# Kernel tuning notes

Hardware: AMD Instinct MI355X
Metric: run time of the kernel (lower is better)

The kernel has to match this reference:

```python
import jax, jax.numpy as jnp
import numpy as np

B, N_PER, D, L, DEG = 16, 2048, 128, 4, 16
N = B * N_PER
E = N * DEG
MSG_EPS = 1e-7  # GENConv message eps


def _lin_init(k, fi, fo):
    kw, kb = jax.random.split(k)
    s = 1.0 / np.sqrt(fi)
    W = jax.random.uniform(kw, (fi, fo), jnp.float32, minval=-s, maxval=s)
    b = jax.random.uniform(kb, (fo,), jnp.float32, minval=-s, maxval=s)
    return W, b


def setup_inputs() -> dict:
    key = jax.random.key(0)
    ks = jax.random.split(key, 6 + 2 * L)
    flat_c = jax.random.normal(ks[0], (N,), jnp.float32)
    edge_weight = jax.random.normal(ks[1], (E,), jnp.float32)
    # edges confined within each graph: local indices + per-graph offset
    e_per = N_PER * DEG
    local = jax.random.randint(ks[2], (2, B, e_per), 0, N_PER, jnp.int32)
    offs = (jnp.arange(B, dtype=jnp.int32) * N_PER)[None, :, None]
    edge_index = (local + offs).reshape(2, E)
    node_W, node_b = _lin_init(ks[3], 1, D)
    edge_W, edge_b = _lin_init(ks[4], 1, D)
    W1l, b1l, W2l, b2l = [], [], [], []
    for i in range(L):
        w1, bb1 = _lin_init(ks[6 + 2 * i], D, 2 * D)
        w2, bb2 = _lin_init(ks[7 + 2 * i], 2 * D, D)
        W1l.append(w1); b1l.append(bb1); W2l.append(w2); b2l.append(bb2)
    lin_W, lin_b = _lin_init(ks[5], D, 1)
    return dict(
        flat_c=flat_c, edge_weight=edge_weight, edge_index=edge_index,
        node_W=node_W, node_b=node_b, edge_W=edge_W, edge_b=edge_b,
        ts=jnp.ones((L,), jnp.float32),
        W1=jnp.stack(W1l), b1=jnp.stack(b1l),
        g1=jnp.ones((L, 2 * D), jnp.float32), be1=jnp.zeros((L, 2 * D), jnp.float32),
        W2=jnp.stack(W2l), b2=jnp.stack(b2l),
        ln_g=jnp.ones((L, D), jnp.float32), ln_b=jnp.zeros((L, D), jnp.float32),
        lin_W=lin_W, lin_b=lin_b)


def _layernorm(x, g, b, eps=1e-5):
    mu = jnp.mean(x, -1, keepdims=True)
    var = jnp.mean((x - mu) ** 2, -1, keepdims=True)
    return (x - mu) * jax.lax.rsqrt(var + eps) * g + b


def _gen_conv(x, edge_attr, src, dst, t, W1, b1, g1, be1, W2, b2):
    # GENConv with softmax aggregation (per-destination, per-channel)
    m = jax.nn.relu(x[src] + edge_attr) + MSG_EPS          # [E, D]
    logits = m * t
    mx = jax.ops.segment_max(logits, dst, num_segments=N)  # [N, D]
    ex = jnp.exp(logits - mx[dst])
    denom = jax.ops.segment_sum(ex, dst, num_segments=N)
    alpha = ex / (denom[dst] + 1e-16)
    aggr = jax.ops.segment_sum(m * alpha, dst, num_segments=N)  # [N, D]
    h = aggr + x
    # MLP: Linear(D,2D) -> LayerNorm -> ReLU -> Linear(2D,D)
    h = jax.nn.relu(_layernorm(h @ W1 + b1, g1, be1))
    return h @ W2 + b2


def reference(flat_c, edge_weight, edge_index, node_W, node_b, edge_W, edge_b,
              ts, W1, b1, g1, be1, W2, b2, ln_g, ln_b, lin_W, lin_b):
    src, dst = edge_index[0], edge_index[1]
    x = flat_c[:, None] @ node_W + node_b              # [N, D]
    ea = edge_weight[:, None] @ edge_W + edge_b        # [E, D]
    # first layer: raw conv only (pre-activation 'res+' scheme)
    x = _gen_conv(x, ea, src, dst, ts[0], W1[0], b1[0], g1[0], be1[0], W2[0], b2[0])
    for l in range(1, L):
        h = x
        z = jax.nn.relu(_layernorm(x, ln_g[l], ln_b[l]))  # dropout=identity (eval)
        x = _gen_conv(z, ea, src, dst, ts[l], W1[l], b1[l], g1[l], be1[l], W2[l], b2[l]) + h
    x = jax.nn.relu(_layernorm(x, ln_g[0], ln_b[0]))
    x = x @ lin_W + lin_b                              # [N, 1]
    out = x.reshape(B, N_PER)                          # equal-size graphs, max_len = N_PER
    return out - out[:, :1]                            # subtract first-node output per graph
```

## Files before the change

kernel.cpp:

```cpp
#include <hip/hip_runtime.h>
#include <hip/hip_bf16.h>
#include <stdint.h>

#define NN   32768
#define EE   524288
#define DD   128
#define D2   256
#define NPER 2048

using f32x4 = __attribute__((ext_vector_type(4))) float;
using sh8   = __attribute__((ext_vector_type(8))) short;
using sh4   = __attribute__((ext_vector_type(4))) short;

__device__ inline uint32_t rtn_hi_bits(float x){
  uint32_t u = __float_as_uint(x);
  return (u + 0x7FFFu + ((u >> 16) & 1u)) & 0xFFFF0000u;
}

__device__ inline int swz_node(int blk, int wave){
  int s = (blk & 7) * 1024 + (blk >> 3);
  return s * 4 + wave;
}

__global__ void k_count(const int* __restrict__ dst, int* __restrict__ cnt){
  int e = blockIdx.x * 256 + threadIdx.x;
  if (e < EE) atomicAdd(&cnt[dst[e]], 1);
}

__global__ __launch_bounds__(1024)
void k_scan(const int* __restrict__ cnt, int* __restrict__ rowptr){
  __shared__ int ps[1024];
  int t = threadIdx.x;
  int loc[32];
  int base = t * 32;
  int s = 0;
  #pragma unroll
  for (int j = 0; j < 32; ++j){ loc[j] = cnt[base + j]; s += loc[j]; }
  ps[t] = s; __syncthreads();
  for (int off = 1; off < 1024; off <<= 1){
    int v = (t >= off) ? ps[t - off] : 0;
    __syncthreads();
    ps[t] += v;
    __syncthreads();
  }
  int run = ps[t] - s;
  #pragma unroll
  for (int j = 0; j < 32; ++j){ rowptr[base + j] = run; run += loc[j]; }
  if (t == 1023) rowptr[NN] = run;
}

__global__ void k_scatter(const int* __restrict__ src, const int* __restrict__ dst,
                          const float* __restrict__ w, const int* __restrict__ rowptr,
                          int* __restrict__ cur, int* __restrict__ es, float* __restrict__ ew){
  int e = blockIdx.x * 256 + threadIdx.x;
  if (e < EE){
    int d = dst[e];
    int pos = rowptr[d] + atomicAdd(&cur[d], 1);
    es[pos] = src[e];
    ew[pos] = w[e];
  }
}

__global__ __launch_bounds__(256)
void k_packw1(const float* __restrict__ W1, ushort* __restrict__ Wh, ushort* __restrict__ Wl){
  int t = blockIdx.x * 256 + threadIdx.x;
  int lane = t & 63, mt = (t >> 6) & 15, kt = (t >> 10) & 3, layer = t >> 12;
  int nl = lane & 15, g = lane >> 4;
  int ucol = mt * 16 + nl;
  const float* Wp = W1 + layer * (DD * D2);
  sh8 hh, ll;
  #pragma unroll
  for (int j = 0; j < 8; ++j){
    int k = kt * 32 + g * 4 + (j & 3) + 16 * (j >> 2);
    float v = Wp[k * D2 + ucol];
    uint32_t hb = rtn_hi_bits(v);
    hh[j] = (short)(hb >> 16);
    ll[j] = (short)(__float_as_uint(v - __uint_as_float(hb)) >> 16);
  }
  *(sh8*)(Wh + t * 8) = hh;
  *(sh8*)(Wl + t * 8) = ll;
}

__global__ __launch_bounds__(256)
void k_packw2(const float* __restrict__ W2, ushort* __restrict__ Wh, ushort* __restrict__ Wl){
  int t = blockIdx.x * 256 + threadIdx.x;
  int lane = t & 63, mt = (t >> 6) & 7, kt = (t >> 9) & 7, layer = t >> 12;
  int nl = lane & 15, g = lane >> 4;
  int xcol = mt * 16 + nl;
  const float* Wp = W2 + layer * (D2 * DD);
  sh8 hh, ll;
  #pragma unroll
  for (int j = 0; j < 8; ++j){
    int k = kt * 32 + g * 4 + (j & 3) + 16 * (j >> 2);
    float v = Wp[k * DD + xcol];
    uint32_t hb = rtn_hi_bits(v);
    hh[j] = (short)(hb >> 16);
    ll[j] = (short)(__float_as_uint(v - __uint_as_float(hb)) >> 16);
  }
  *(sh8*)(Wh + t * 8) = hh;
  *(sh8*)(Wl + t * 8) = ll;
}

__global__ __launch_bounds__(256)
void k_encode(const float* __restrict__ c, const float* __restrict__ nW,
              const float* __restrict__ nb, float* __restrict__ Z){
  int n  = swz_node(blockIdx.x, threadIdx.x >> 6);
  int d0 = (threadIdx.x & 63) * 2;
  float cv = c[n];
  float2 o;
  o.x = cv * nW[d0]     + nb[d0];
  o.y = cv * nW[d0 + 1] + nb[d0 + 1];
  *(float2*)(Z + (size_t)n * DD + d0) = o;
}

__global__ __launch_bounds__(256)
void k_edge(const float* __restrict__ Z, const int* __restrict__ rowptr,
            const int* __restrict__ es, const float* __restrict__ ew,
            const float* __restrict__ eW, const float* __restrict__ eB,
            const float* __restrict__ ts, int layer,
            ushort* __restrict__ Hh, ushort* __restrict__ Hl){
  int n  = swz_node(blockIdx.x, threadIdx.x >> 6);
  int ld = threadIdx.x & 63;
  int d0 = ld * 2;
  float t  = ts[layer];
  float wx = eW[d0], wy = eW[d0 + 1];
  float bx = eB[d0], by = eB[d0 + 1];
  int r0 = rowptr[n], r1 = rowptr[n + 1];
  int deg = r1 - r0;
  int dcap = deg < 64 ? deg : 64;

  int   se = 0; float we = 0.f;
  if (ld < deg){ se = es[r0 + ld]; we = ew[r0 + ld]; }

  float m0r = -1e30f, m1r = -1e30f;
  float s0a = 0.f, s1a = 0.f, a0a = 0.f, a1a = 0.f;

  auto body = [&](float2 zc, float wj){
    float m0 = fmaxf(zc.x + fmaf(wj, wx, bx), 0.f) + 1e-7f;
    float m1 = fmaxf(zc.y + fmaf(wj, wy, by), 0.f) + 1e-7f;
    float l0 = m0 * t, l1 = m1 * t;
    if (__builtin_expect(l0 > m0r + 8.f || l1 > m1r + 8.f, 0)){
      float n0 = fmaxf(m0r, l0), n1 = fmaxf(m1r, l1);
      float e0 = __expf(m0r - n0), e1 = __expf(m1r - n1);
      s0a *= e0; a0a *= e0; m0r = n0;
      s1a *= e1; a1a *= e1; m1r = n1;
    }
    float p0 = __expf(l0 - m0r), p1 = __expf(l1 - m1r);
    s0a += p0; a0a = fmaf(p0, m0, a0a);
    s1a += p1; a1a = fmaf(p1, m1, a1a);
  };

  float2 z0 = make_float2(0.f, 0.f), z1 = make_float2(0.f, 0.f);
  float  wA = 0.f, wB = 0.f;
  if (dcap > 0){
    int s0i = __shfl(se, 0); wA = __shfl(we, 0);
    z0 = *(const float2*)(Z + (size_t)s0i * DD + d0);
  }
  if (dcap > 1){
    int s1i = __shfl(se, 1); wB = __shfl(we, 1);
    z1 = *(const float2*)(Z + (size_t)s1i * DD + d0);
  }
  for (int j = 0; j < dcap; ++j){
    float2 zc = z0; float wj = wA;
    z0 = z1; wA = wB;
    if (j + 2 < dcap){
      int sn = __shfl(se, j + 2); wB = __shfl(we, j + 2);
      z1 = *(const float2*)(Z + (size_t)sn * DD + d0);
    }
    body(zc, wj);
  }
  for (int e = r0 + 64; e < r1; ++e){
    int   s = es[e];
    float w = ew[e];
    float2 zc = *(const float2*)(Z + (size_t)s * DD + d0);
    body(zc, w);
  }

  float2 zn = *(const float2*)(Z + (size_t)n * DD + d0);
  float hx = a0a / (s0a + 1e-16f) + zn.x;
  float hy = a1a / (s1a + 1e-16f) + zn.y;
  uint32_t hbx = rtn_hi_bits(hx), hby = rtn_hi_bits(hy);
  uint32_t hw = (hbx >> 16) | (hby & 0xFFFF0000u);
  float lx = hx - __uint_as_float(hbx), ly = hy - __uint_as_float(hby);
  uint32_t lw = (__float_as_uint(lx) >> 16) | (__float_as_uint(ly) & 0xFFFF0000u);
  ((uint32_t*)(Hh + (size_t)n * DD))[ld] = hw;
  ((uint32_t*)(Hl + (size_t)n * DD))[ld] = lw;
}

__global__ __launch_bounds__(256, 2)
void k_mlp(const ushort* __restrict__ Hhi, const ushort* __restrict__ Hlo,
           const ushort* __restrict__ W1h, const ushort* __restrict__ W1l,
           const float* __restrict__ b1, const float* __restrict__ g1,
           const float* __restrict__ be1,
           const ushort* __restrict__ W2h, const ushort* __restrict__ W2l,
           const float* __restrict__ b2, const float* __restrict__ Xres,
           float* __restrict__ Xout,
           const float* __restrict__ lnG, const float* __restrict__ lnB,
           float* __restrict__ Zout, int hasRes, int writeX)
{
  __shared__ ushort Ufh[16384];
  __shared__ ushort Ufl[16384];
  __shared__ float2 Pln[256];

  const int tid = threadIdx.x;
  const int w = tid >> 6, l = tid & 63, nl = l & 15, g = l >> 4;
  const int bs = (blockIdx.x & 7) * 64 + (blockIdx.x >> 3);
  const int n0 = bs * 64;

  f32x4 acc[4][4];
  #pragma unroll
  for (int mi = 0; mi < 4; ++mi)
    #pragma unroll
    for (int nt = 0; nt < 4; ++nt) acc[mi][nt] = (f32x4)0.f;

  const int hbase = (n0 + nl) * DD + g * 4;

  #pragma unroll
  for (int kt = 0; kt < 4; ++kt){
    sh8 ah[4], al[4];
    #pragma unroll
    for (int mi = 0; mi < 4; ++mi){
      int fi = ((kt * 16 + w * 4 + mi) * 64 + l) * 8;
      ah[mi] = *(const sh8*)(W1h + fi);
      al[mi] = *(const sh8*)(W1l + fi);
    }
    sh8 bh[4], bl[4];
    #pragma unroll
    for (int nt = 0; nt < 4; ++nt){
      int hi_ = hbase + nt * 16 * DD + kt * 32;
      sh8 vh, vl;
      ((sh4*)&vh)[0] = *(const sh4*)(Hhi + hi_);
      ((sh4*)&vh)[1] = *(const sh4*)(Hhi + hi_ + 16);
      ((sh4*)&vl)[0] = *(const sh4*)(Hlo + hi_);
      ((sh4*)&vl)[1] = *(const sh4*)(Hlo + hi_ + 16);
      bh[nt] = vh; bl[nt] = vl;
    }
    #pragma unroll
    for (int mi = 0; mi < 4; ++mi)
      #pragma unroll
      for (int nt = 0; nt < 4; ++nt){
        acc[mi][nt] = __builtin_amdgcn_mfma_f32_16x16x32_bf16(ah[mi], bh[nt], acc[mi][nt], 0, 0, 0);
        acc[mi][nt] = __builtin_amdgcn_mfma_f32_16x16x32_bf16(ah[mi], bl[nt], acc[mi][nt], 0, 0, 0);
        acc[mi][nt] = __builtin_amdgcn_mfma_f32_16x16x32_bf16(al[mi], bh[nt], acc[mi][nt], 0, 0, 0);
      }
  }

  #pragma unroll
  for (int mi = 0; mi < 4; ++mi){
    f32x4 bv = *(const f32x4*)(b1 + w * 64 + mi * 16 + g * 4);
    #pragma unroll
    for (int nt = 0; nt < 4; ++nt) acc[mi][nt] += bv;
  }
  float s1[4], s2[4];
  #pragma unroll
  for (int nt = 0; nt < 4; ++nt){
    float a = 0.f, b = 0.f;
    #pragma unroll
    for (int mi = 0; mi < 4; ++mi)
      #pragma unroll
      for (int r = 0; r < 4; ++r){ float v = acc[mi][nt][r]; a += v; b += v * v; }
    a += __shfl_xor(a, 16); b += __shfl_xor(b, 16);
    a += __shfl_xor(a, 32); b += __shfl_xor(b, 32);
    s1[nt] = a; s2[nt] = b;
  }
  {
    float p1 = (g == 0) ? s1[0] : (g == 1) ? s1[1] : (g == 2) ? s1[2] : s1[3];
    float p2 = (g == 0) ? s2[0] : (g == 1) ? s2[1] : (g == 2) ? s2[2] : s2[3];
    Pln[(g * 16 + nl) * 4 + w] = make_float2(p1, p2);
  }
  __syncthreads();

  {
    f32x4 gv[4], ev[4];
    #pragma unroll
    for (int mi = 0; mi < 4; ++mi){
      gv[mi] = *(const f32x4*)(g1  + w * 64 + mi * 16 + g * 4);
      ev[mi] = *(const f32x4*)(be1 + w * 64 + mi * 16 + g * 4);
    }
    #pragma unroll
    for (int nt = 0; nt < 4; ++nt){
      int node = nt * 16 + nl;
      float t1 = 0.f, t2 = 0.f;
      #pragma unroll
      for (int wi = 0; wi < 4; ++wi){
        float2 pp = Pln[node * 4 + wi];
        t1 += pp.x; t2 += pp.y;
      }
      float mean = t1 * (1.f / D2);
      float var  = t2 * (1.f / D2) - mean * mean;
      float rstd = 1.f / sqrtf(var + 1e-5f);
      #pragma unroll
      for (int p = 0; p < 2; ++p){
        sh8 uh, ul;
        #pragma unroll
        for (int j = 0; j < 8; ++j){
          int mi = 2 * p + (j >> 2), r = j & 3;
          float v = (acc[mi][nt][r] - mean) * rstd * gv[mi][r] + ev[mi][r];
          v = fmaxf(v, 0.f);
          uint32_t hb = rtn_hi_bits(v);
          uh[j] = (short)(hb >> 16);
          ul[j] = (short)(__float_as_uint(v - __uint_as_float(hb)) >> 16);
        }
        int fo = (((2 * w + p) * 4 + nt) * 64 + l) * 8;
        *(sh8*)(Ufh + fo) = uh;
        *(sh8*)(Ufl + fo) = ul;
      }
    }
  }
  __syncthreads();

  f32x4 a2[2][4];
  #pragma unroll
  for (int mi = 0; mi < 2; ++mi)
    #pragma unroll
    for (int nt = 0; nt < 4; ++nt) a2[mi][nt] = (f32x4)0.f;
  #pragma unroll
  for (int kt = 0; kt < 8; ++kt){
    sh8 wh[2], wl[2];
    #pragma unroll
    for (int mi = 0; mi < 2; ++mi){
      int fi = ((kt * 8 + w * 2 + mi) * 64 + l) * 8;
      wh[mi] = *(const sh8*)(W2h + fi);
      wl[mi] = *(const sh8*)(W2l + fi);
    }
    sh8 uh[4], ul[4];
    #pragma unroll
    for (int nt = 0; nt < 4; ++nt){
      int fo = ((kt * 4 + nt) * 64 + l) * 8;
      uh[nt] = *(const sh8*)(Ufh + fo);
      ul[nt] = *(const sh8*)(Ufl + fo);
    }
    #pragma unroll
    for (int mi = 0; mi < 2; ++mi)
      #pragma unroll
      for (int nt = 0; nt < 4; ++nt){
        a2[mi][nt] = __builtin_amdgcn_mfma_f32_16x16x32_bf16(wh[mi], uh[nt], a2[mi][nt], 0, 0, 0);
        a2[mi][nt] = __builtin_amdgcn_mfma_f32_16x16x32_bf16(wh[mi], ul[nt], a2[mi][nt], 0, 0, 0);
        a2[mi][nt] = __builtin_amdgcn_mfma_f32_16x16x32_bf16(wl[mi], uh[nt], a2[mi][nt], 0, 0, 0);
      }
  }
  __syncthreads();

  float* Xb = (float*)Ufh;
  #pragma unroll
  for (int mi = 0; mi < 2; ++mi)
    #pragma unroll
    for (int nt = 0; nt < 4; ++nt){
      int node = nt * 16 + nl;
      int xc = (w * 2 + mi) * 16 + g * 4;
      int idx = node * DD + (xc ^ ((node & 7) << 2));
      *(f32x4*)(Xb + idx) = a2[mi][nt];
    }
  __syncthreads();

  {
    int en = tid >> 2, ec = tid & 3;
    f32x4 vr[8];
    float s1e = 0.f, s2e = 0.f;
    #pragma unroll
    for (int i = 0; i < 8; ++i){
      int q = ec + i * 4;
      int c = q * 4;
      int idx = en * DD + ((q ^ (en & 7)) << 2);
      f32x4 v = *(const f32x4*)(Xb + idx);
      v += *(const f32x4*)(b2 + c);
      if (hasRes) v += *(const f32x4*)(Xres + (size_t)(n0 + en) * DD + c);
      vr[i] = v;
      #pragma unroll
      for (int r = 0; r < 4; ++r){ s1e += v[r]; s2e += v[r] * v[r]; }
    }
    s1e += __shfl_xor(s1e, 1); s2e += __shfl_xor(s2e, 1);
    s1e += __shfl_xor(s1e, 2); s2e += __shfl_xor(s2e, 2);
    float mean = s1e * (1.f / DD);
    float var  = s2e * (1.f / DD) - mean * mean;
    float rs   = 1.f / sqrtf(var + 1e-5f);
    #pragma unroll
    for (int i = 0; i < 8; ++i){
      int q = ec + i * 4;
      int c = q * 4;
      if (writeX) *(f32x4*)(Xout + (size_t)(n0 + en) * DD + c) = vr[i];
      f32x4 gv = *(const f32x4*)(lnG + c);
      f32x4 bv = *(const f32x4*)(lnB + c);
      f32x4 z;
      #pragma unroll
      for (int r = 0; r < 4; ++r)
        z[r] = fmaxf((vr[i][r] - mean) * rs * gv[r] + bv[r], 0.f);
      *(f32x4*)(Zout + (size_t)(n0 + en) * DD + c) = z;
    }
  }
}

__global__ __launch_bounds__(256)
void k_fin1(const float* __restrict__ Zf, const float* __restrict__ linW,
            const float* __restrict__ linb, float* __restrict__ y){
  int n  = swz_node(blockIdx.x, threadIdx.x >> 6);
  int d0 = (threadIdx.x & 63) * 2;
  float2 v = *(const float2*)(Zf + (size_t)n * DD + d0);
  float p = v.x * linW[d0] + v.y * linW[d0 + 1];
  #pragma unroll
  for (int m = 1; m < 64; m <<= 1) p += __shfl_xor(p, m);
  if ((threadIdx.x & 63) == 0) y[n] = p + linb[0];
}

__global__ void k_fin2(const float* __restrict__ y, float* __restrict__ out){
  int i = blockIdx.x * 256 + threadIdx.x;
  out[i] = y[i] - y[i & ~(NPER - 1)];
}

extern "C" void kernel_launch(void* const* d_in, const int* in_sizes, int n_in,
                              void* d_out, int out_size, void* d_ws, size_t ws_size,
                              hipStream_t stream){
  const float* flat_c = (const float*)d_in[0];
  const float* edge_w = (const float*)d_in[1];
  const int*   eidx   = (const int*)  d_in[2];
  const float* nodeW  = (const float*)d_in[3];
  const float* nodeB  = (const float*)d_in[4];
  const float* edgeW  = (const float*)d_in[5];
  const float* edgeB  = (const float*)d_in[6];
  const float* ts     = (const float*)d_in[7];
  const float* W1     = (const float*)d_in[8];
  const float* b1     = (const float*)d_in[9];
  const float* g1     = (const float*)d_in[10];
  const float* be1    = (const float*)d_in[11];
  const float* W2     = (const float*)d_in[12];
  const float* b2     = (const float*)d_in[13];
  const float* lng    = (const float*)d_in[14];
  const float* lnb    = (const float*)d_in[15];
  const float* linW   = (const float*)d_in[16];
  const float* linb   = (const float*)d_in[17];
  float* out = (float*)d_out;

  char* wsp = (char*)d_ws;
  size_t off = 0;
  auto alloc = [&](size_t bytes) -> void* {
    void* p = wsp + off;
    off += (bytes + 255) & ~(size_t)255;
    return p;
  };
  float*  bufA = (float*) alloc((size_t)NN * DD * 4);
  float*  bufB = (float*) alloc((size_t)NN * DD * 4);
  ushort* Hhi  = (ushort*)alloc((size_t)NN * DD * 2);
  ushort* Hlo  = (ushort*)alloc((size_t)NN * DD * 2);
  ushort* W1h  = (ushort*)alloc((size_t)4 * 32768 * 2);
  ushort* W1l  = (ushort*)alloc((size_t)4 * 32768 * 2);
  ushort* W2h  = (ushort*)alloc((size_t)4 * 32768 * 2);
  ushort* W2l  = (ushort*)alloc((size_t)4 * 32768 * 2);
  int*   cnt   = (int*)  alloc((size_t)NN * 4);
  int*   rowpt = (int*)  alloc((size_t)(NN + 1) * 4);
  int*   cur   = (int*)  alloc((size_t)NN * 4);
  int*   es    = (int*)  alloc((size_t)EE * 4);
  float* ewS   = (float*)alloc((size_t)EE * 4);
  float* y     = (float*)alloc((size_t)NN * 4);
  if (off > ws_size) return;

  const int* srcI = eidx;
  const int* dstI = eidx + EE;

  (void)hipMemsetAsync(cnt, 0, (size_t)NN * 4, stream);
  (void)hipMemsetAsync(cur, 0, (size_t)NN * 4, stream);
  k_count  <<<EE / 256, 256, 0, stream>>>(dstI, cnt);
  k_scan   <<<1, 1024, 0, stream>>>(cnt, rowpt);
  k_scatter<<<EE / 256, 256, 0, stream>>>(srcI, dstI, edge_w, rowpt, cur, es, ewS);

  k_packw1<<<64, 256, 0, stream>>>(W1, W1h, W1l);
  k_packw2<<<64, 256, 0, stream>>>(W2, W2h, W2l);

  k_encode<<<NN / 4, 256, 0, stream>>>(flat_c, nodeW, nodeB, bufA);
  for (int l = 0; l < 4; ++l){
    k_edge<<<NN / 4, 256, 0, stream>>>(bufA, rowpt, es, ewS, edgeW, edgeB, ts, l, Hhi, Hlo);
    int nx = (l + 1) & 3;
    k_mlp <<<NN / 64, 256, 0, stream>>>(Hhi, Hlo,
                                        W1h + (size_t)l * 32768, W1l + (size_t)l * 32768,
                                        b1 + l * D2, g1 + l * D2, be1 + l * D2,
                                        W2h + (size_t)l * 32768, W2l + (size_t)l * 32768,
                                        b2 + l * DD, bufB, bufB,
                                        lng + nx * DD, lnb + nx * DD, bufA,
                                        l > 0 ? 1 : 0, l < 3 ? 1 : 0);
  }
  k_fin1<<<NN / 4, 256, 0, stream>>>(bufA, linW, linb, y);
  k_fin2<<<NN / 256, 256, 0, stream>>>(y, out);
}
```

Baseline: 363.1 us.

## Fuse node encoding into first edge pass, merge packing, memset and final kernels

Layer 0's edge kernel now rebuilds source-node features on the fly from the scalar input and the node linear weights, so the encode kernel and its full feature-matrix write and gather are gone. The two weight-packing kernels become one launch, the two memsets become one by placing the counters next to each other, and the final projection and per-graph subtraction become one kernel that subtracts the first node's features before the dot product, which also drops the bias. The edge gather loop is restructured to prefetch four neighbours at a time. These changes cut launches and memory traffic, but the added template specialisation could raise register use.

```diff
diff --git a/kernel.cpp b/kernel.cpp
--- a/kernel.cpp
+++ b/kernel.cpp
@@ -62,59 +62,51 @@
 }
 
 __global__ __launch_bounds__(256)
-void k_packw1(const float* __restrict__ W1, ushort* __restrict__ Wh, ushort* __restrict__ Wl){
-  int t = blockIdx.x * 256 + threadIdx.x;
-  int lane = t & 63, mt = (t >> 6) & 15, kt = (t >> 10) & 3, layer = t >> 12;
-  int nl = lane & 15, g = lane >> 4;
-  int ucol = mt * 16 + nl;
-  const float* Wp = W1 + layer * (DD * D2);
-  sh8 hh, ll;
-  #pragma unroll
-  for (int j = 0; j < 8; ++j){
-    int k = kt * 32 + g * 4 + (j & 3) + 16 * (j >> 2);
-    float v = Wp[k * D2 + ucol];
-    uint32_t hb = rtn_hi_bits(v);
-    hh[j] = (short)(hb >> 16);
-    ll[j] = (short)(__float_as_uint(v - __uint_as_float(hb)) >> 16);
-  }
-  *(sh8*)(Wh + t * 8) = hh;
-  *(sh8*)(Wl + t * 8) = ll;
-}
-
+void k_packw(const float* __restrict__ W1, const float* __restrict__ W2,
+             ushort* __restrict__ W1h, ushort* __restrict__ W1l,
+             ushort* __restrict__ W2h, ushort* __restrict__ W2l){
+  if (blockIdx.x < 64){
+    int t = blockIdx.x * 256 + threadIdx.x;
+    int lane = t & 63, mt = (t >> 6) & 15, kt = (t >> 10) & 3, layer = t >> 12;
+    int nl = lane & 15, g = lane >> 4;
+    int ucol = mt * 16 + nl;
+    const float* Wp = W1 + layer * (DD * D2);
+    sh8 hh, ll;
+    #pragma unroll
+    for (int j = 0; j < 8; ++j){
+      int k = kt * 32 + g * 4 + (j & 3) + 16 * (j >> 2);
+      float v = Wp[k * D2 + ucol];
+      uint32_t hb = rtn_hi_bits(v);
+      hh[j] = (short)(hb >> 16);
+      ll[j] = (short)(__float_as_uint(v - __uint_as_float(hb)) >> 16);
+    }
+    *(sh8*)(W1h + t * 8) = hh;
+    *(sh8*)(W1l + t * 8) = ll;
+  } else {
+    int t = (blockIdx.x - 64) * 256 + threadIdx.x;
+    int lane = t & 63, mt = (t >> 6) & 7, kt = (t >> 9) & 7, layer = t >> 12;
+    int nl = lane & 15, g = lane >> 4;
+    int xcol = mt * 16 + nl;
+    const float* Wp = W2 + layer * (D2 * DD);
+    sh8 hh, ll;
+    #pragma unroll
+    for (int j = 0; j < 8; ++j){
+      int k = kt * 32 + g * 4 + (j & 3) + 16 * (j >> 2);
+      float v = Wp[k * DD + xcol];
+      uint32_t hb = rtn_hi_bits(v);
+      hh[j] = (short)(hb >> 16);
+      ll[j] = (short)(__float_as_uint(v - __uint_as_float(hb)) >> 16);
+    }
+    *(sh8*)(W2h + t * 8) = hh;
+    *(sh8*)(W2l + t * 8) = ll;
+  }
+}
+
+template<int MODE>
 __global__ __launch_bounds__(256)
-void k_packw2(const float* __restrict__ W2, ushort* __restrict__ Wh, ushort* __restrict__ Wl){
-  int t = blockIdx.x * 256 + threadIdx.x;
-  int lane = t & 63, mt = (t >> 6) & 7, kt = (t >> 9) & 7, layer = t >> 12;
-  int nl = lane & 15, g = lane >> 4;
-  int xcol = mt * 16 + nl;
-  const float* Wp = W2 + layer * (D2 * DD);
-  sh8 hh, ll;
-  #pragma unroll
-  for (int j = 0; j < 8; ++j){
-    int k = kt * 32 + g * 4 + (j & 3) + 16 * (j >> 2);
-    float v = Wp[k * DD + xcol];
-    uint32_t hb = rtn_hi_bits(v);
-    hh[j] = (short)(hb >> 16);
-    ll[j] = (short)(__float_as_uint(v - __uint_as_float(hb)) >> 16);
-  }
-  *(sh8*)(Wh + t * 8) = hh;
-  *(sh8*)(Wl + t * 8) = ll;
-}
-
-__global__ __launch_bounds__(256)
-void k_encode(const float* __restrict__ c, const float* __restrict__ nW,
-              const float* __restrict__ nb, float* __restrict__ Z){
-  int n  = swz_node(blockIdx.x, threadIdx.x >> 6);
-  int d0 = (threadIdx.x & 63) * 2;
-  float cv = c[n];
-  float2 o;
-  o.x = cv * nW[d0]     + nb[d0];
-  o.y = cv * nW[d0 + 1] + nb[d0 + 1];
-  *(float2*)(Z + (size_t)n * DD + d0) = o;
-}
-
-__global__ __launch_bounds__(256)
-void k_edge(const float* __restrict__ Z, const int* __restrict__ rowptr,
+void k_edge(const float* __restrict__ Zf, const float* __restrict__ cvec,
+            const float* __restrict__ nW, const float* __restrict__ nb,
+            const int* __restrict__ rowptr,
             const int* __restrict__ es, const float* __restrict__ ew,
             const float* __restrict__ eW, const float* __restrict__ eB,
             const float* __restrict__ ts, int layer,
@@ -125,16 +117,34 @@
   float t  = ts[layer];
   float wx = eW[d0], wy = eW[d0 + 1];
   float bx = eB[d0], by = eB[d0 + 1];
+  float nwx = 0.f, nwy = 0.f, nbx = 0.f, nby = 0.f;
+  if (MODE == 0){ nwx = nW[d0]; nwy = nW[d0 + 1]; nbx = nb[d0]; nby = nb[d0 + 1]; }
   int r0 = rowptr[n], r1 = rowptr[n + 1];
   int deg = r1 - r0;
   int dcap = deg < 64 ? deg : 64;
 
-  int   se = 0; float we = 0.f;
-  if (ld < deg){ se = es[r0 + ld]; we = ew[r0 + ld]; }
+  int se = 0; float we = 0.f, ce = 0.f;
+  if (ld < deg){
+    se = es[r0 + ld]; we = ew[r0 + ld];
+    if (MODE == 0) ce = cvec[se];
+  }
 
   float m0r = -1e30f, m1r = -1e30f;
   float s0a = 0.f, s1a = 0.f, a0a = 0.f, a1a = 0.f;
 
+  auto fetchz = [&](int j, float2& z, float& wv){
+    if (j < dcap){
+      wv = __shfl(we, j);
+      if (MODE == 0){
+        float cs = __shfl(ce, j);
+        z.x = fmaf(cs, nwx, nbx);
+        z.y = fmaf(cs, nwy, nby);
+      } else {
+        int s = __shfl(se, j);
+        z = *(const float2*)(Zf + (size_t)s * DD + d0);
+      }
+    }
+  };
   auto body = [&](float2 zc, float wj){
     float m0 = fmaxf(zc.x + fmaf(wj, wx, bx), 0.f) + 1e-7f;
     float m1 = fmaxf(zc.y + fmaf(wj, wy, by), 0.f) + 1e-7f;
@@ -150,35 +160,42 @@
     s1a += p1; a1a = fmaf(p1, m1, a1a);
   };
 
-  float2 z0 = make_float2(0.f, 0.f), z1 = make_float2(0.f, 0.f);
-  float  wA = 0.f, wB = 0.f;
-  if (dcap > 0){
-    int s0i = __shfl(se, 0); wA = __shfl(we, 0);
-    z0 = *(const float2*)(Z + (size_t)s0i * DD + d0);
-  }
-  if (dcap > 1){
-    int s1i = __shfl(se, 1); wB = __shfl(we, 1);
-    z1 = *(const float2*)(Z + (size_t)s1i * DD + d0);
-  }
-  for (int j = 0; j < dcap; ++j){
-    float2 zc = z0; float wj = wA;
-    z0 = z1; wA = wB;
-    if (j + 2 < dcap){
-      int sn = __shfl(se, j + 2); wB = __shfl(we, j + 2);
-      z1 = *(const float2*)(Z + (size_t)sn * DD + d0);
-    }
-    body(zc, wj);
+  float2 zc0 = {0,0}, zc1 = {0,0}, zc2 = {0,0}, zc3 = {0,0};
+  float  wc0 = 0.f, wc1 = 0.f, wc2 = 0.f, wc3 = 0.f;
+  fetchz(0, zc0, wc0); fetchz(1, zc1, wc1); fetchz(2, zc2, wc2); fetchz(3, zc3, wc3);
+  for (int base = 0; base < dcap; base += 4){
+    float2 zn0 = {0,0}, zn1 = {0,0}, zn2 = {0,0}, zn3 = {0,0};
+    float  wn0 = 0.f, wn1 = 0.f, wn2 = 0.f, wn3 = 0.f;
+    fetchz(base + 4, zn0, wn0); fetchz(base + 5, zn1, wn1);
+    fetchz(base + 6, zn2, wn2); fetchz(base + 7, zn3, wn3);
+    body(zc0, wc0);
+    if (base + 1 < dcap) body(zc1, wc1);
+    if (base + 2 < dcap) body(zc2, wc2);
+    if (base + 3 < dcap) body(zc3, wc3);
+    zc0 = zn0; wc0 = wn0; zc1 = zn1; wc1 = wn1;
+    zc2 = zn2; wc2 = wn2; zc3 = zn3; wc3 = wn3;
   }
   for (int e = r0 + 64; e < r1; ++e){
-    int   s = es[e];
-    float w = ew[e];
-    float2 zc = *(const float2*)(Z + (size_t)s * DD + d0);
+    float2 zc; float w = ew[e];
+    if (MODE == 0){
+      float cs = cvec[es[e]];
+      zc.x = fmaf(cs, nwx, nbx); zc.y = fmaf(cs, nwy, nby);
+    } else {
+      zc = *(const float2*)(Zf + (size_t)es[e] * DD + d0);
+    }
     body(zc, w);
   }
 
-  float2 zn = *(const float2*)(Z + (size_t)n * DD + d0);
-  float hx = a0a / (s0a + 1e-16f) + zn.x;
-  float hy = a1a / (s1a + 1e-16f) + zn.y;
+  float znx, zny;
+  if (MODE == 0){
+    float cn = cvec[n];
+    znx = fmaf(cn, nwx, nbx); zny = fmaf(cn, nwy, nby);
+  } else {
+    float2 zn2 = *(const float2*)(Zf + (size_t)n * DD + d0);
+    znx = zn2.x; zny = zn2.y;
+  }
+  float hx = a0a / (s0a + 1e-16f) + znx;
+  float hy = a1a / (s1a + 1e-16f) + zny;
   uint32_t hbx = rtn_hi_bits(hx), hby = rtn_hi_bits(hy);
   uint32_t hw = (hbx >> 16) | (hby & 0xFFFF0000u);
   float lx = hx - __uint_as_float(hbx), ly = hy - __uint_as_float(hby);
@@ -391,20 +408,18 @@
 }
 
 __global__ __launch_bounds__(256)
-void k_fin1(const float* __restrict__ Zf, const float* __restrict__ linW,
-            const float* __restrict__ linb, float* __restrict__ y){
+void k_fin(const float* __restrict__ Zf, const float* __restrict__ linW,
+           float* __restrict__ out){
   int n  = swz_node(blockIdx.x, threadIdx.x >> 6);
   int d0 = (threadIdx.x & 63) * 2;
-  float2 v = *(const float2*)(Zf + (size_t)n * DD + d0);
-  float p = v.x * linW[d0] + v.y * linW[d0 + 1];
+  int nb_ = n & ~(NPER - 1);
+  float2 v  = *(const float2*)(Zf + (size_t)n  * DD + d0);
+  float2 vb = *(const float2*)(Zf + (size_t)nb_ * DD + d0);
+  float2 lw = *(const float2*)(linW + d0);
+  float p = (v.x - vb.x) * lw.x + (v.y - vb.y) * lw.y;
   #pragma unroll
   for (int m = 1; m < 64; m <<= 1) p += __shfl_xor(p, m);
-  if ((threadIdx.x & 63) == 0) y[n] = p + linb[0];
-}
-
-__global__ void k_fin2(const float* __restrict__ y, float* __restrict__ out){
-  int i = blockIdx.x * 256 + threadIdx.x;
-  out[i] = y[i] - y[i & ~(NPER - 1)];
+  if ((threadIdx.x & 63) == 0) out[n] = p;
 }
 
 extern "C" void kernel_launch(void* const* d_in, const int* in_sizes, int n_in,
@@ -427,7 +442,6 @@
   const float* lng    = (const float*)d_in[14];
   const float* lnb    = (const float*)d_in[15];
   const float* linW   = (const float*)d_in[16];
-  const float* linb   = (const float*)d_in[17];
   float* out = (float*)d_out;
 
   char* wsp = (char*)d_ws;
@@ -446,28 +460,28 @@
   ushort* W2h  = (ushort*)alloc((size_t)4 * 32768 * 2);
   ushort* W2l  = (ushort*)alloc((size_t)4 * 32768 * 2);
   int*   cnt   = (int*)  alloc((size_t)NN * 4);
+  int*   cur   = (int*)  alloc((size_t)NN * 4);
   int*   rowpt = (int*)  alloc((size_t)(NN + 1) * 4);
-  int*   cur   = (int*)  alloc((size_t)NN * 4);
   int*   es    = (int*)  alloc((size_t)EE * 4);
   float* ewS   = (float*)alloc((size_t)EE * 4);
-  float* y     = (float*)alloc((size_t)NN * 4);
   if (off > ws_size) return;
 
   const int* srcI = eidx;
   const int* dstI = eidx + EE;
 
-  (void)hipMemsetAsync(cnt, 0, (size_t)NN * 4, stream);
-  (void)hipMemsetAsync(cur, 0, (size_t)NN * 4, stream);
+  (void)hipMemsetAsync(cnt, 0, (size_t)2 * NN * 4, stream);
   k_count  <<<EE / 256, 256, 0, stream>>>(dstI, cnt);
   k_scan   <<<1, 1024, 0, stream>>>(cnt, rowpt);
   k_scatter<<<EE / 256, 256, 0, stream>>>(srcI, dstI, edge_w, rowpt, cur, es, ewS);
-
-  k_packw1<<<64, 256, 0, stream>>>(W1, W1h, W1l);
-  k_packw2<<<64, 256, 0, stream>>>(W2, W2h, W2l);
-
-  k_encode<<<NN / 4, 256, 0, stream>>>(flat_c, nodeW, nodeB, bufA);
+  k_packw  <<<128, 256, 0, stream>>>(W1, W2, W1h, W1l, W2h, W2l);
+
   for (int l = 0; l < 4; ++l){
-    k_edge<<<NN / 4, 256, 0, stream>>>(bufA, rowpt, es, ewS, edgeW, edgeB, ts, l, Hhi, Hlo);
+    if (l == 0)
+      k_edge<0><<<NN / 4, 256, 0, stream>>>(nullptr, flat_c, nodeW, nodeB,
+                                            rowpt, es, ewS, edgeW, edgeB, ts, l, Hhi, Hlo);
+    else
+      k_edge<1><<<NN / 4, 256, 0, stream>>>(bufA, nullptr, nullptr, nullptr,
+                                            rowpt, es, ewS, edgeW, edgeB, ts, l, Hhi, Hlo);
     int nx = (l + 1) & 3;
     k_mlp <<<NN / 64, 256, 0, stream>>>(Hhi, Hlo,
                                         W1h + (size_t)l * 32768, W1l + (size_t)l * 32768,
@@ -477,6 +491,5 @@
                                         lng + nx * DD, lnb + nx * DD, bufA,
                                         l > 0 ? 1 : 0, l < 3 ? 1 : 0);
   }
-  k_fin1<<<NN / 4, 256, 0, stream>>>(bufA, linW, linb, y);
-  k_fin2<<<NN / 256, 256, 0, stream>>>(y, out);
-}
+  k_fin<<<NN / 4, 256, 0, stream>>>(bufA, linW, out);
+}
```

Result: no change. 360.1 us (-0.8%).
